# Kernel tuning notes

Hardware: AMD Instinct MI355X
Metric: run time of the kernel (lower is better)

## Reference

```python
import jax, jax.numpy as jnp
import numpy as np

NUM_GROUPS = 32
EPS = 1e-6


def group_norm(x, gamma, beta):
    # x: (B, C, H, W)
    B, C, H, W = x.shape
    g = x.reshape(B, NUM_GROUPS, C // NUM_GROUPS, H, W)
    mean = g.mean(axis=(2, 3, 4), keepdims=True)
    var = g.var(axis=(2, 3, 4), keepdims=True)
    g = (g - mean) / jnp.sqrt(var + EPS)
    g = g.reshape(B, C, H, W)
    return g * gamma[None, :, None, None] + beta[None, :, None, None]


def nin(x, W, b):
    # 1x1 linear projection over channel dim
    return jnp.einsum('bchw,cd->bdhw', x, W) + b[None, :, None, None]


def setup_inputs() -> dict:
    key = jax.random.key(0)
    ks = jax.random.split(key, 8)
    B, C, H, W = 32, 512, 32, 32
    lim = np.sqrt(3 * 0.1 / C)  # NIN init_scale=0.1 uniform limit
    return {
        'x': jax.random.normal(ks[0], (B, C, H, W), jnp.float32),
        'gamma': jnp.ones((C,), jnp.float32),
        'beta': jnp.zeros((C,), jnp.float32),
        'Wq': jax.random.uniform(ks[1], (C, C), jnp.float32, -lim, lim),
        'bq': jnp.zeros((C,), jnp.float32),
        'Wk': jax.random.uniform(ks[2], (C, C), jnp.float32, -lim, lim),
        'bk': jnp.zeros((C,), jnp.float32),
        'Wv': jax.random.uniform(ks[3], (C, C), jnp.float32, -lim, lim),
        'bv': jnp.zeros((C,), jnp.float32),
        'Wp': jax.random.normal(ks[4], (C, C), jnp.float32) * 1e-5,  # init_scale=0.0 -> ~0
        'bp': jnp.zeros((C,), jnp.float32),
    }


def reference(x, gamma, beta, Wq, bq, Wk, bk, Wv, bv, Wp, bp):
    B, C, H, W = x.shape
    h = group_norm(x, gamma, beta)
    q = nin(h, Wq, bq)
    k = nin(h, Wk, bk)
    v = nin(h, Wv, bv)
    # full (HW)x(HW) attention weights, as the original materializes
    w = jnp.einsum('bchw,bcHW->bhwHW', q, k) * (C ** -0.5)
    w = w.reshape(B, H, W, H * W)
    w = jax.nn.softmax(w, axis=-1)
    w = w.reshape(B, H, W, H, W)
    h_out = jnp.einsum('bhwHW,bcHW->bchw', w, v)
    h_out = nin(h_out, Wp, bp)
    return x + h_out
```

## Files before the change

kernel.cpp:

```cpp
#include <hip/hip_runtime.h>
#include <hip/hip_bf16.h>
#include <math.h>

typedef __attribute__((ext_vector_type(8))) short bf16x8;
typedef __attribute__((ext_vector_type(4))) float f32x4;

typedef const __attribute__((address_space(1))) unsigned int guint;
typedef __attribute__((address_space(3))) unsigned int luint;

static __device__ __forceinline__ short f2bf(float f) {
    union { float f; unsigned u; } a; a.f = f;
    unsigned r = 0x7FFFu + ((a.u >> 16) & 1u);
    return (short)((a.u + r) >> 16);
}
static __device__ __forceinline__ float bf2f(short s) {
    union { unsigned u; float f; } a;
    a.u = ((unsigned)(unsigned short)s) << 16;
    return a.f;
}

__global__ __launch_bounds__(256)
void transpose_w(const float* __restrict__ w0, const float* __restrict__ w1,
                 const float* __restrict__ w2, const float* __restrict__ w3,
                 short* __restrict__ outT, float qscale)
{
    __shared__ float ld[32][33];
    const float* W = (blockIdx.z == 0) ? w0 : (blockIdx.z == 1) ? w1
                   : (blockIdx.z == 2) ? w2 : w3;
    const float sc = (blockIdx.z == 0) ? qscale : 1.f;
    short* O = outT + (long long)blockIdx.z * 512 * 512;
    const int tx = threadIdx.x & 31, ty = threadIdx.x >> 5;
    const int c0 = blockIdx.y * 32, d0 = blockIdx.x * 32;
#pragma unroll
    for (int r = 0; r < 4; ++r)
        ld[ty + 8 * r][tx] = W[(long long)(c0 + ty + 8 * r) * 512 + d0 + tx];
    __syncthreads();
#pragma unroll
    for (int r = 0; r < 4; ++r)
        O[(long long)(d0 + ty + 8 * r) * 512 + c0 + tx] = f2bf(ld[tx][ty + 8 * r] * sc);
}

__global__ __launch_bounds__(256)
void concat_bias(const float* __restrict__ bq, const float* __restrict__ bk,
                 float* __restrict__ bqk, float qscale)
{
    int i = blockIdx.x * 256 + threadIdx.x;
    bqk[i] = (i < 512) ? bq[i] * qscale : bk[i - 512];
}

__global__ __launch_bounds__(256)
void gn_stats(const float* __restrict__ x, float2* __restrict__ stats)
{
    const int bg = blockIdx.x;
    const float4* p = reinterpret_cast<const float4*>(x + (long long)bg * 16384);
    float s = 0.f, ss = 0.f;
    for (int i = threadIdx.x; i < 4096; i += 256) {
        float4 v = p[i];
        s  += v.x + v.y + v.z + v.w;
        ss += v.x * v.x + v.y * v.y + v.z * v.z + v.w * v.w;
    }
    __shared__ float rs[256], rss[256];
    rs[threadIdx.x] = s; rss[threadIdx.x] = ss;
    __syncthreads();
    for (int o = 128; o > 0; o >>= 1) {
        if (threadIdx.x < o) { rs[threadIdx.x] += rs[threadIdx.x + o];
                               rss[threadIdx.x] += rss[threadIdx.x + o]; }
        __syncthreads();
    }
    if (threadIdx.x == 0) {
        float mean = rs[0] * (1.f / 16384.f);
        float var  = rss[0] * (1.f / 16384.f) - mean * mean;
        stats[bg] = make_float2(mean, rsqrtf(var + 1e-6f));
    }
}

__global__ __launch_bounds__(256)
void gn_apply_t(const float* __restrict__ x, const float2* __restrict__ stats,
                const float* __restrict__ gamma, const float* __restrict__ beta,
                short* __restrict__ hn)
{
    __shared__ short lds[32 * 520];
    const int t = threadIdx.x;
    const int s0 = blockIdx.x * 32;
    const int b  = blockIdx.y;
#pragma unroll
    for (int i = 0; i < 16; ++i) {
        int qi = t + 256 * i;
        int c = qi >> 3, sc = qi & 7;
        float4 v = *reinterpret_cast<const float4*>(
            x + ((long long)(b * 512 + c)) * 1024 + s0 + sc * 4);
        float2 st = stats[b * 32 + (c >> 4)];
        float ga = gamma[c], be = beta[c];
        float m = st.x, r = st.y;
        lds[(sc * 4 + 0) * 520 + c] = f2bf((v.x - m) * r * ga + be);
        lds[(sc * 4 + 1) * 520 + c] = f2bf((v.y - m) * r * ga + be);
        lds[(sc * 4 + 2) * 520 + c] = f2bf((v.z - m) * r * ga + be);
        lds[(sc * 4 + 3) * 520 + c] = f2bf((v.w - m) * r * ga + be);
    }
    __syncthreads();
#pragma unroll
    for (int i = 0; i < 8; ++i) {
        int p = t + 256 * i;
        int s = p >> 6, j = p & 63;
        float4 v = *reinterpret_cast<const float4*>(&lds[s * 520 + j * 8]);
        *reinterpret_cast<float4*>(
            hn + ((long long)(b * 1024 + s0 + s)) * 512 + j * 8) = v;
    }
}

template<int BIAS_M, int BIAS_N, int RESID, int EXPOUT, int DIVROW>
__global__ __launch_bounds__(512, 2)
void nt_gemm(const short* __restrict__ A, const short* __restrict__ B,
             void* __restrict__ Cv,
             const float* __restrict__ biasM, const float* __restrict__ biasN,
             const float* __restrict__ resid, const float* __restrict__ rs,
             int rsM, float scale, int K, int lda, int ldb, int ldc,
             long long sA, long long sB, long long sC,
             int tilesM, int tilesPerBatch)
{
    __shared__ short lsA[2][2][128 * 64];
    __shared__ short lsB[2][2][128 * 64];

    const int id = blockIdx.x;
    const int chunk = gridDim.x >> 3;
    const int gid = (id & 7) * chunk + (id >> 3);
    const int bz = gid / tilesPerBatch;
    const int tt = gid - bz * tilesPerBatch;
    const int m0 = (tt % tilesM) * 256;
    const int n0 = (tt / tilesM) * 256;

    const int t = threadIdx.x;
    const int lane = t & 63;
    const int w = t >> 6;
    const int wrs = w >> 1;
    const int wcs = w & 1;
    const int lr16 = lane & 15, lkg = lane >> 4;
    const int sw = lr16 & 7;

    const int srow = t >> 3;
    const int scol = ((t & 7) ^ (srow & 7)) * 8;
    const short* gA = A + (long long)bz * sA + (long long)(m0 + srow) * lda + scol;
    const short* gB = B + (long long)bz * sB + (long long)(n0 + srow) * ldb + scol;

    f32x4 acc[4][2][4];
#pragma unroll
    for (int q = 0; q < 4; ++q)
#pragma unroll
        for (int i = 0; i < 2; ++i)
#pragma unroll
            for (int j = 0; j < 4; ++j) acc[q][i][j] = (f32x4){0.f, 0.f, 0.f, 0.f};

    const int nk = K >> 6;

#define STAGE_A(buf, h, kt)                                                    \
    {                                                                          \
        _Pragma("unroll")                                                      \
        for (int c = 0; c < 2; ++c)                                            \
            __builtin_amdgcn_global_load_lds(                                  \
                (guint*)(gA + (long long)((h) * 128 + 64 * c) * lda + (kt) * 64), \
                (luint*)&lsA[buf][h][t * 8 + 4096 * c], 16, 0, 0);             \
    }
#define STAGE_B(buf, h, kt)                                                    \
    {                                                                          \
        _Pragma("unroll")                                                      \
        for (int c = 0; c < 2; ++c)                                            \
            __builtin_amdgcn_global_load_lds(                                  \
                (guint*)(gB + (long long)((h) * 128 + 64 * c) * ldb + (kt) * 64), \
                (luint*)&lsB[buf][h][t * 8 + 4096 * c], 16, 0, 0);             \
    }

#define LDA_HALF(buf, h)                                                       \
    _Pragma("unroll")                                                          \
    for (int mi2 = 0; mi2 < 2; ++mi2)                                          \
        _Pragma("unroll")                                                      \
        for (int ks = 0; ks < 2; ++ks)                                         \
            af[mi2][ks] = *reinterpret_cast<const bf16x8*>(                    \
                &lsA[buf][h][(wrs * 32 + mi2 * 16 + lr16) * 64 +               \
                             (((ks * 4 + lkg) ^ sw) * 8)]);
#define LDB_HALF(buf, h)                                                       \
    _Pragma("unroll")                                                          \
    for (int ni = 0; ni < 4; ++ni)                                             \
        _Pragma("unroll")                                                      \
        for (int ks = 0; ks < 2; ++ks)                                         \
            bfr[ni][ks] = *reinterpret_cast<const bf16x8*>(                    \
                &lsB[buf][h][(wcs * 64 + ni * 16 + lr16) * 64 +                \
                             (((ks * 4 + lkg) ^ sw) * 8)]);

#define PH_SYNC                                                                \
    __builtin_amdgcn_s_barrier();                                              \
    asm volatile("s_waitcnt lgkmcnt(0)" ::: "memory");                         \
    __builtin_amdgcn_sched_barrier(0)
#define PH_CLOSE                                                               \
    __builtin_amdgcn_sched_barrier(0);                                         \
    __builtin_amdgcn_s_barrier()

#define MFMAQ(q)                                                               \
    __builtin_amdgcn_s_setprio(1);                                             \
    _Pragma("unroll")                                                          \
    for (int ks = 0; ks < 2; ++ks)                                             \
        _Pragma("unroll")                                                      \
        for (int mi2 = 0; mi2 < 2; ++mi2)                                      \
            _Pragma("unroll")                                                  \
            for (int ni = 0; ni < 4; ++ni)                                     \
                acc[q][mi2][ni] = __builtin_amdgcn_mfma_f32_16x16x32_bf16(     \
                    af[mi2][ks], bfr[ni][ks], acc[q][mi2][ni], 0, 0, 0);       \
    __builtin_amdgcn_s_setprio(0)

#define FRAME(b, kt)                                                           \
    {                                                                          \
        bf16x8 af[2][2], bfr[4][2];                                            \
                                                      \
        LDA_HALF(b, 0) LDB_HALF(b, 0)                                          \
        STAGE_A((b) ^ 1, 0, (kt) + 1);                                         \
        PH_SYNC;                                                               \
        MFMAQ(0);                                                              \
        PH_CLOSE;                                                              \
                                   \
        LDA_HALF(b, 1)                                                         \
        STAGE_B((b) ^ 1, 1, (kt) + 1);                                         \
        PH_SYNC;                                                               \
        MFMAQ(2);                                                              \
        PH_CLOSE;                                                              \
                                   \
        LDB_HALF(b, 1)                                                         \
        STAGE_B(b, 0, (kt) + 2);                                               \
        PH_SYNC;                                                               \
        MFMAQ(3);                                                              \
        PH_CLOSE;                                                              \
                      \
        LDA_HALF(b, 0)                                                         \
        STAGE_A(b, 1, (kt) + 2);                                               \
        PH_SYNC;                                                               \
        MFMAQ(1);                                                              \
        __builtin_amdgcn_sched_barrier(0);                                     \
        asm volatile("s_waitcnt vmcnt(4)" ::: "memory");                       \
        PH_CLOSE;                                                              \
    }

    STAGE_A(0, 0, 0); STAGE_B(0, 0, 0); STAGE_A(0, 1, 0); STAGE_B(0, 1, 0);
    STAGE_B(1, 0, 1); STAGE_A(1, 1, 1);
    asm volatile("s_waitcnt vmcnt(4)" ::: "memory");
    __builtin_amdgcn_sched_barrier(0);
    __builtin_amdgcn_s_barrier();

    for (int kt = 0; kt < nk; kt += 2) {
        FRAME(0, kt)
        FRAME(1, kt + 1)
    }
#undef STAGE_A
#undef STAGE_B
#undef LDA_HALF
#undef LDB_HALF
#undef PH_SYNC
#undef PH_CLOSE
#undef MFMAQ
#undef FRAME

#pragma unroll
    for (int ah = 0; ah < 2; ++ah) {
#pragma unroll
        for (int bh = 0; bh < 2; ++bh) {
#pragma unroll
            for (int mi2 = 0; mi2 < 2; ++mi2) {
                float addm[4], mul[4];
#pragma unroll
                for (int j = 0; j < 4; ++j) {
                    const int rrow = m0 + ah * 128 + wrs * 32 + mi2 * 16 + lkg * 4 + j;
                    addm[j] = BIAS_M ? biasM[rrow] : 0.f;
                    mul[j]  = DIVROW ? 1.f / rs[(long long)bz * rsM + rrow] : 1.f;
                }
#pragma unroll
                for (int ni = 0; ni < 4; ++ni) {
                    const int col = n0 + bh * 128 + wcs * 64 + ni * 16 + lr16;
                    float bn = BIAS_N ? biasN[col] : 0.f;
#pragma unroll
                    for (int j = 0; j < 4; ++j) {
                        const int rrow = m0 + ah * 128 + wrs * 32 + mi2 * 16 + lkg * 4 + j;
                        float v2 = acc[ah * 2 + bh][mi2][ni][j] + addm[j] + bn;
                        v2 *= scale;
                        if (EXPOUT) v2 = __expf(v2 - 8.f);
                        if (DIVROW) v2 *= mul[j];
                        const long long idx = (long long)rrow * ldc + col;
                        if (RESID) {
                            float* Cf = (float*)Cv + (long long)bz * sC;
                            Cf[idx] = v2 + resid[(long long)bz * sC + idx];
                        } else {
                            short* Cs = (short*)Cv + (long long)bz * sC;
                            Cs[idx] = f2bf(v2);
                        }
                    }
                }
            }
        }
    }
}

__global__ __launch_bounds__(256)
void rowsum_rows(const short* __restrict__ S, float* __restrict__ rs)
{
    const int wave = threadIdx.x >> 6, lane = threadIdx.x & 63;
    const long long row = (long long)blockIdx.x * 4 + wave;
    const short* p = S + row * 1024;
    bf16x8 h0 = *reinterpret_cast<const bf16x8*>(p + lane * 8);
    bf16x8 h1 = *reinterpret_cast<const bf16x8*>(p + 512 + lane * 8);
    float s = 0.f;
#pragma unroll
    for (int j = 0; j < 8; ++j) s += bf2f(h0[j]) + bf2f(h1[j]);
#pragma unroll
    for (int o = 32; o > 0; o >>= 1) s += __shfl_xor(s, o);
    if (lane == 0) rs[row] = s;
}

extern "C" void kernel_launch(void* const* d_in, const int* in_sizes, int n_in,
                              void* d_out, int out_size, void* d_ws, size_t ws_size,
                              hipStream_t stream)
{
    (void)in_sizes; (void)n_in; (void)out_size; (void)ws_size;
    const float* x     = (const float*)d_in[0];
    const float* gamma = (const float*)d_in[1];
    const float* beta  = (const float*)d_in[2];
    const float* Wq = (const float*)d_in[3];
    const float* bq = (const float*)d_in[4];
    const float* Wk = (const float*)d_in[5];
    const float* bk = (const float*)d_in[6];
    const float* Wv = (const float*)d_in[7];
    const float* bv = (const float*)d_in[8];
    const float* Wp = (const float*)d_in[9];
    const float* bp = (const float*)d_in[10];
    float* out = (float*)d_out;

    char* ws = (char*)d_ws;
    short*  expS = (short*)ws;
    short*  hn   = (short*)ws;
    short*  qkb  = (short*)(ws + (64LL << 20));
    short*  vbuf = (short*)(ws + (128LL << 20));
    short*  wT   = (short*)(ws + (160LL << 20));
    float2* stats = (float2*)(ws + (162LL << 20));
    float*  bqk   = (float*)(ws + (162LL << 20) + (16 << 10));
    float*  rs    = (float*)(ws + (162LL << 20) + (32 << 10));
    short*  ho    = qkb;

    const short* WqkT = wT;
    const short* WvT  = wT + 2 * 512 * 512;
    const short* WpT  = wT + 3 * 512 * 512;

    const float qscale = 0.044194173824159216f;

    transpose_w<<<dim3(16, 16, 4), 256, 0, stream>>>(Wq, Wk, Wv, Wp, wT, qscale);
    concat_bias<<<dim3(4), 256, 0, stream>>>(bq, bk, bqk, qscale);
    gn_stats<<<dim3(1024), 256, 0, stream>>>(x, stats);
    gn_apply_t<<<dim3(32, 32), 256, 0, stream>>>(x, stats, gamma, beta, hn);

    nt_gemm<0, 1, 0, 0, 0><<<512, 512, 0, stream>>>(
        hn, WqkT, qkb, nullptr, bqk, nullptr, nullptr, 0, 1.f,
        512, 512, 512, 1024, 1024 * 512, 0, 1024LL * 1024, 4, 16);
    nt_gemm<1, 0, 0, 0, 0><<<256, 512, 0, stream>>>(
        WvT, hn, vbuf, bv, nullptr, nullptr, nullptr, 0, 1.f,
        512, 512, 512, 1024, 0, 1024 * 512, 512 * 1024, 2, 8);
    nt_gemm<0, 0, 0, 1, 0><<<512, 512, 0, stream>>>(
        qkb, qkb + 512, expS, nullptr, nullptr, nullptr, nullptr, 0, 1.f,
        512, 1024, 1024, 1024, 1024LL * 1024, 1024LL * 1024, 1024LL * 1024, 4, 16);
    rowsum_rows<<<dim3(8192), 256, 0, stream>>>(expS, rs);
    nt_gemm<0, 0, 0, 0, 1><<<256, 512, 0, stream>>>(
        expS, vbuf, ho, nullptr, nullptr, nullptr, rs, 1024, 1.f,
        1024, 1024, 1024, 512, 1024LL * 1024, 512 * 1024, 1024 * 512, 4, 8);
    nt_gemm<1, 0, 1, 0, 0><<<256, 512, 0, stream>>>(
        WpT, ho, out, bp, nullptr, x, nullptr, 0, 1.f,
        512, 512, 512, 1024, 0, 1024 * 512, 512LL * 1024, 2, 8);
}
```

Measured before the change: 234.6 us.

## Restructure GEMM main loop into two-phase schedule with fewer barriers

Replaces the four-phase frame, which had eight barriers per k-tile, with a two-phase frame. Each phase loads the LDS fragments for A and B halves into separate register sets and reuses the B fragments across both A halves. Global-to-LDS prefetch of the next tile is issued earlier and tracked with vmcnt waits, in place of barrier-bracketed phases. The goal is to cut synchronisation overhead and let more MFMAs run between barriers. The cost is higher register pressure and a possible LDS race if the vmcnt accounting is wrong.

Result: no change. 231.2 us (-1.5%).

```diff
diff --git a/kernel.cpp b/kernel.cpp
--- a/kernel.cpp
+++ b/kernel.cpp
@@ -169,33 +169,28 @@
                 (luint*)&lsB[buf][h][t * 8 + 4096 * c], 16, 0, 0);             \
     }
 
-#define LDA_HALF(buf, h)                                                       \
+#define LDA_HALF(dst, buf, h)                                                  \
     _Pragma("unroll")                                                          \
     for (int mi2 = 0; mi2 < 2; ++mi2)                                          \
         _Pragma("unroll")                                                      \
         for (int ks = 0; ks < 2; ++ks)                                         \
-            af[mi2][ks] = *reinterpret_cast<const bf16x8*>(                    \
+            dst[mi2][ks] = *reinterpret_cast<const bf16x8*>(                   \
                 &lsA[buf][h][(wrs * 32 + mi2 * 16 + lr16) * 64 +               \
                              (((ks * 4 + lkg) ^ sw) * 8)]);
-#define LDB_HALF(buf, h)                                                       \
+#define LDB_HALF(dst, buf, h)                                                  \
     _Pragma("unroll")                                                          \
     for (int ni = 0; ni < 4; ++ni)                                             \
         _Pragma("unroll")                                                      \
         for (int ks = 0; ks < 2; ++ks)                                         \
-            bfr[ni][ks] = *reinterpret_cast<const bf16x8*>(                    \
+            dst[ni][ks] = *reinterpret_cast<const bf16x8*>(                    \
                 &lsB[buf][h][(wcs * 64 + ni * 16 + lr16) * 64 +                \
                              (((ks * 4 + lkg) ^ sw) * 8)]);
 
-#define PH_SYNC                                                                \
-    __builtin_amdgcn_s_barrier();                                              \
+#define LGKM0                                                                  \
     asm volatile("s_waitcnt lgkmcnt(0)" ::: "memory");                         \
     __builtin_amdgcn_sched_barrier(0)
-#define PH_CLOSE                                                               \
-    __builtin_amdgcn_sched_barrier(0);                                         \
-    __builtin_amdgcn_s_barrier()
-
-#define MFMAQ(q)                                                               \
-    __builtin_amdgcn_s_setprio(1);                                             \
+
+#define MFMAQ(q, Af, Bf)                                                       \
     _Pragma("unroll")                                                          \
     for (int ks = 0; ks < 2; ++ks)                                             \
         _Pragma("unroll")                                                      \
@@ -203,43 +198,45 @@
             _Pragma("unroll")                                                  \
             for (int ni = 0; ni < 4; ++ni)                                     \
                 acc[q][mi2][ni] = __builtin_amdgcn_mfma_f32_16x16x32_bf16(     \
-                    af[mi2][ks], bfr[ni][ks], acc[q][mi2][ni], 0, 0, 0);       \
-    __builtin_amdgcn_s_setprio(0)
+                    Af[mi2][ks], Bf[ni][ks], acc[q][mi2][ni], 0, 0, 0);
 
 #define FRAME(b, kt)                                                           \
     {                                                                          \
-        bf16x8 af[2][2], bfr[4][2];                                            \
-                                                      \
-        LDA_HALF(b, 0) LDB_HALF(b, 0)                                          \
+        bf16x8 a0[2][2], a1[2][2], b0f[4][2], b1f[4][2];                       \
+                                \
+        LDB_HALF(b0f, b, 0)                                                    \
+        LDA_HALF(a0, b, 0)                                                     \
+        STAGE_B((b) ^ 1, 0, (kt) + 1);                                         \
+        STAGE_B((b) ^ 1, 1, (kt) + 1);                                         \
         STAGE_A((b) ^ 1, 0, (kt) + 1);                                         \
-        PH_SYNC;                                                               \
-        MFMAQ(0);                                                              \
-        PH_CLOSE;                                                              \
-                                   \
-        LDA_HALF(b, 1)                                                         \
-        STAGE_B((b) ^ 1, 1, (kt) + 1);                                         \
-        PH_SYNC;                                                               \
-        MFMAQ(2);                                                              \
-        PH_CLOSE;                                                              \
-                                   \
-        LDB_HALF(b, 1)                                                         \
-        STAGE_B(b, 0, (kt) + 2);                                               \
-        PH_SYNC;                                                               \
-        MFMAQ(3);                                                              \
-        PH_CLOSE;                                                              \
-                      \
-        LDA_HALF(b, 0)                                                         \
-        STAGE_A(b, 1, (kt) + 2);                                               \
-        PH_SYNC;                                                               \
-        MFMAQ(1);                                                              \
+        LGKM0;                                                                 \
+        LDB_HALF(b1f, b, 1)                                                    \
+        __builtin_amdgcn_s_setprio(1);                                         \
+        MFMAQ(0, a0, b0f)                                                      \
+        __builtin_amdgcn_s_setprio(0);                                         \
+        LGKM0;                                                                 \
+        __builtin_amdgcn_s_setprio(1);                                         \
+        MFMAQ(1, a0, b1f)                                                      \
+        __builtin_amdgcn_s_setprio(0);                                         \
         __builtin_amdgcn_sched_barrier(0);                                     \
-        asm volatile("s_waitcnt vmcnt(4)" ::: "memory");                       \
-        PH_CLOSE;                                                              \
-    }
-
-    STAGE_A(0, 0, 0); STAGE_B(0, 0, 0); STAGE_A(0, 1, 0); STAGE_B(0, 1, 0);
-    STAGE_B(1, 0, 1); STAGE_A(1, 1, 1);
-    asm volatile("s_waitcnt vmcnt(4)" ::: "memory");
+        asm volatile("s_waitcnt vmcnt(6)" ::: "memory");                       \
+        __builtin_amdgcn_s_barrier();                                          \
+              \
+        LDA_HALF(a1, b, 1)                                                     \
+        STAGE_A((b) ^ 1, 1, (kt) + 1);                                         \
+        LGKM0;                                                                 \
+        __builtin_amdgcn_s_setprio(1);                                         \
+        MFMAQ(2, a1, b0f)                                                      \
+        MFMAQ(3, a1, b1f)                                                      \
+        __builtin_amdgcn_s_setprio(0);                                         \
+        __builtin_amdgcn_sched_barrier(0);                                     \
+        asm volatile("s_waitcnt vmcnt(2)" ::: "memory");                       \
+        __builtin_amdgcn_s_barrier();                                          \
+    }
+
+    STAGE_B(0, 0, 0); STAGE_B(0, 1, 0); STAGE_A(0, 0, 0);
+    STAGE_A(0, 1, 0);
+    asm volatile("s_waitcnt vmcnt(2)" ::: "memory");
     __builtin_amdgcn_sched_barrier(0);
     __builtin_amdgcn_s_barrier();
 
@@ -251,8 +248,7 @@
 #undef STAGE_B
 #undef LDA_HALF
 #undef LDB_HALF
-#undef PH_SYNC
-#undef PH_CLOSE
+#undef LGKM0
 #undef MFMAQ
 #undef FRAME
 
```
